# Optimization experiments

Hardware: AMD Instinct MI355X
Metric: run time of the kernel (lower is better)

Reference implementation:

```python
import jax, jax.numpy as jnp
import numpy as np
import math

DN = ('NCHW', 'OIHW', 'NCHW')
TOTAL_STRIDE = 8.0
SCORE_OFFSET = 3.0
SCORE_SIZE = 25
BN_EPS = 1e-5


def conv2d(x, w, b, pad):
    y = jax.lax.conv_general_dilated(x, w, (1, 1), [(pad, pad), (pad, pad)],
                                     dimension_numbers=DN)
    return y + b[None, :, None, None]


def conv_module(x, w1, b1, ws, bs):
    x = conv2d(x, w1, b1, 1)
    for i in range(ws.shape[0]):
        x = conv2d(jax.nn.relu(x), ws[i], bs[i], 1)
    return x


def bn_eval(x, g, b):
    # inference-mode BatchNorm2d: running_mean=0, running_var=1
    s = g / jnp.sqrt(1.0 + BN_EPS)
    return x * s[None, :, None, None] + b[None, :, None, None]


def memory_read(fm, fq):
    B, C, T, H, W = fm.shape
    fm_flat = fm.reshape(B, C, T * H * W)          # (B, C, THW)
    fq_flat = fq.reshape(B, C, H * W)              # (B, C, HW)
    # scores: (B, THW, HW), softmax over the memory axis (THW)
    w = jnp.einsum('bct,bcq->btq', fm_flat, fq_flat) / math.sqrt(512.0)
    w = jax.nn.softmax(w, axis=1)
    mem = jnp.einsum('bct,btq->bcq', fm_flat, w).reshape(B, C, H, W)
    return jnp.concatenate([mem, fq], axis=1)      # (B, 2C, H, W)


def fm_ctr():
    gx = SCORE_OFFSET + TOTAL_STRIDE * jnp.arange(SCORE_SIZE, dtype=jnp.float32)[None, :]
    gy = SCORE_OFFSET + TOTAL_STRIDE * jnp.arange(SCORE_SIZE, dtype=jnp.float32)[:, None]
    return jnp.stack([jnp.broadcast_to(gx, (SCORE_SIZE, SCORE_SIZE)),
                      jnp.broadcast_to(gy, (SCORE_SIZE, SCORE_SIZE))], axis=-1)  # (H,W,2)


def reference(fm, fq, cls1_w, cls1_b, clsk_w, clsk_b, reg1_w, reg1_b, regk_w, regk_b,
              w_cls, b_cls, g_cls, be_cls, w_ctr, b_ctr, g_ctr, be_ctr,
              w_off, b_off, g_off, be_off, si, bi):
    y = memory_read(fm, fq)
    cls_feat = conv_module(y, cls1_w, cls1_b, clsk_w, clsk_b)
    reg_feat = conv_module(y, reg1_w, reg1_b, regk_w, regk_b)
    cls_score = bn_eval(conv2d(cls_feat, w_cls, b_cls, 0), g_cls, be_cls)  # (B,1,H,W)
    ctr_score = bn_eval(conv2d(cls_feat, w_ctr, b_ctr, 0), g_ctr, be_ctr)  # (B,1,H,W)
    offsets = bn_eval(conv2d(reg_feat, w_off, b_off, 0), g_off, be_off)    # (B,4,H,W)

    B = cls_score.shape[0]
    cls_score = cls_score.transpose(0, 2, 3, 1).reshape(B, -1, 1)
    ctr_score = ctr_score.transpose(0, 2, 3, 1).reshape(B, -1, 1)
    offsets = jnp.exp(si * offsets + bi) * TOTAL_STRIDE

    ctr = fm_ctr()                                  # (H,W,2)
    off = offsets.transpose(0, 2, 3, 1)             # (B,H,W,4)
    xy0 = ctr[None] - off[..., :2]
    xy1 = ctr[None] + off[..., 2:]
    bbox = jnp.concatenate([xy0, xy1], axis=-1).reshape(B, -1, 4)
    return cls_score, ctr_score, bbox


def setup_inputs() -> dict:
    key = jax.random.key(0)
    ks = jax.random.split(key, 16)
    B, C, T, H, W = 8, 20, 24, 25, 25
    WSC = 0.02  # small conv-weight scale to keep the 7-conv stack + exp() stable
    inp = {
        'fm': jax.random.normal(ks[0], (B, C, T, H, W), jnp.float32),
        'fq': jax.random.normal(ks[1], (B, C, H, W), jnp.float32),
        'cls1_w': jax.random.normal(ks[2], (256, 40, 3, 3), jnp.float32) * WSC,
        'cls1_b': jnp.zeros((256,), jnp.float32),
        'clsk_w': jax.random.normal(ks[3], (6, 256, 256, 3, 3), jnp.float32) * WSC,
        'clsk_b': jnp.zeros((6, 256), jnp.float32),
        'reg1_w': jax.random.normal(ks[4], (256, 40, 3, 3), jnp.float32) * WSC,
        'reg1_b': jnp.zeros((256,), jnp.float32),
        'regk_w': jax.random.normal(ks[5], (6, 256, 256, 3, 3), jnp.float32) * WSC,
        'regk_b': jnp.zeros((6, 256), jnp.float32),
        'w_cls': jax.random.normal(ks[6], (1, 256, 1, 1), jnp.float32) * WSC,
        'b_cls': jnp.zeros((1,), jnp.float32),
        'g_cls': jnp.ones((1,), jnp.float32),
        'be_cls': jnp.zeros((1,), jnp.float32),
        'w_ctr': jax.random.normal(ks[7], (1, 256, 1, 1), jnp.float32) * WSC,
        'b_ctr': jnp.zeros((1,), jnp.float32),
        'g_ctr': jnp.ones((1,), jnp.float32),
        'be_ctr': jnp.zeros((1,), jnp.float32),
        'w_off': jax.random.normal(ks[8], (4, 256, 1, 1), jnp.float32) * WSC,
        'b_off': jnp.zeros((4,), jnp.float32),
        'g_off': jnp.ones((4,), jnp.float32),
        'be_off': jnp.zeros((4,), jnp.float32),
        'si': jnp.float32(1.0),
        'bi': jnp.float32(0.0),
    }
    return inp
```

## Files before the change

kernel.cpp:

```cpp
#include <hip/hip_runtime.h>
#include <math.h>

#define BATCH 8
#define CCH 20
#define THW 15000
#define HW 625
#define SSIDE 25
#define PHW 729

#define NKEY 15000
#define TPAD 15104
#define NKT 118
#define NKC 20
#define KCHUNK 6

typedef __attribute__((ext_vector_type(8))) short bf16x8;
typedef __attribute__((ext_vector_type(4))) float f32x4;

#define YBF_OFF  0ULL
#define XA_OFF   746496ULL
#define XB_OFF   6718464ULL
#define WT0_OFF  12690432ULL
#define WT_OFF   13280256ULL
#define WTL_ELEMS 1179648ULL
#define FMT_OFF  27436032ULL
#define FM32_OFF 35169280ULL
#define FQB_OFF  42902528ULL
#define PART_OFF 43230208ULL

__device__ __forceinline__ ushort f2bf(float x) {
    unsigned u = __float_as_uint(x);
    u = (u + 0x7FFFu + ((u >> 16) & 1u)) >> 16;
    return (ushort)u;
}
__device__ __forceinline__ float bf2f(ushort v) {
    return __uint_as_float(((unsigned)v) << 16);
}

__device__ __forceinline__ void gload16(const void* g, void* l) {
    __builtin_amdgcn_global_load_lds((const __attribute__((address_space(1))) void*)g,
                                     (__attribute__((address_space(3))) void*)l, 16, 0, 0);
}

__global__ __launch_bounds__(256) void prep_fm(const float* __restrict__ fm,
                                               ushort* __restrict__ fmbT,
                                               ushort* __restrict__ fmb32) {
    __shared__ ushort sT2[256][34];
    const int tid = threadIdx.x;
    const int t0 = blockIdx.x * 256;
    const int b = blockIdx.y;
    const int t = t0 + tid;
    #pragma unroll 4
    for (int c = 0; c < CCH; c++) {
        float v = (t < NKEY) ? fm[((size_t)b * CCH + c) * THW + t] : 0.f;
        ushort h = f2bf(v);
        sT2[tid][c] = h;
        fmb32[((size_t)b * 32 + c) * TPAD + t] = h;
    }
    #pragma unroll
    for (int cz = CCH; cz < 32; cz++)
        fmb32[((size_t)b * 32 + cz) * TPAD + t] = 0;
    __syncthreads();
    const int g = tid >> 4, j = tid & 15;
    uint* dstb = (uint*)fmbT + ((size_t)b * TPAD + t0) * 16 + j;
    #pragma unroll
    for (int i = 0; i < 16; i++) {
        int r = g + 16 * i;
        uint v = 0;
        if (j < 10) v = *(const uint*)&sT2[r][2 * j];
        dstb[(size_t)r * 16] = v;
    }
}

__global__ __launch_bounds__(256) void prep_fq(const float* __restrict__ fq,
                                               ushort* __restrict__ fqb) {
    int idx = blockIdx.x * 256 + threadIdx.x;
    if (idx >= BATCH * 640) return;
    int b = idx / 640, q = idx % 640;
    const float qscale = 1.4426950408889634f * 0.04419417382415922f;
    ushort* dst = fqb + (size_t)idx * 32;
    #pragma unroll 4
    for (int c = 0; c < CCH; c++) {
        float v = (q < HW) ? fq[((size_t)b * CCH + c) * HW + q] * qscale : 0.f;
        dst[c] = f2bf(v);
    }
    #pragma unroll
    for (int c = CCH; c < 32; c++) dst[c] = 0;
}

__global__ __launch_bounds__(512) void attn_flash(const ushort* __restrict__ fmbT,
                                                  const ushort* __restrict__ fmb32,
                                                  const ushort* __restrict__ fqb,
                                                  char* __restrict__ part) {
    __shared__ __align__(16) ushort sK[2][4096];
    __shared__ __align__(16) ushort sV[2][4096];
    __shared__ __align__(16) ushort sP[8][2048];
    const int tid = threadIdx.x;
    const int wave = tid >> 6, lane = tid & 63;
    const int q16 = lane & 15, quad = lane >> 4;
    const int phys = blockIdx.x;
    const int lid = (phys & 7) * 60 + (phys >> 3);
    const int b = lid / 60;
    const int rem = lid - b * 60;
    const int kc = rem / 3;
    const int xq = rem - kc * 3;
    const int qt0 = xq * 2 + (wave >> 2);
    const bool act = (qt0 < 5);
    const int qt = act ? qt0 : 4;
    const int wq = wave & 3;

    bf16x8 Qf[2];
    #pragma unroll
    for (int nf = 0; nf < 2; nf++)
        Qf[nf] = *(const bf16x8*)(fqb + ((size_t)(b * 640 + qt * 128 + wq * 32 + nf * 16 + q16) << 5) + quad * 8);

    f32x4 O[2][2];
    #pragma unroll
    for (int nf = 0; nf < 2; nf++) { O[nf][0] = (f32x4)0.f; O[nf][1] = (f32x4)0.f; }
    float lp0 = 0.f, lp1 = 0.f;
    const f32x4 zz = (f32x4)0.f;

    const int kt0 = kc * KCHUNK;
    const int kt1 = (kt0 + KCHUNK < NKT) ? kt0 + KCHUNK : NKT;

    const int rK = tid >> 2, cK = tid & 3;
    const int rV = tid >> 4, cV = tid & 15;
    const ushort* srcK = fmbT + ((size_t)(b * TPAD + rK) << 5) + ((cK ^ (rK & 3)) << 3);
    const ushort* srcV = fmb32 + (size_t)(b * 32 + rV) * TPAD + ((cV ^ (rV & 7)) << 3);
    auto stage = [&](int kt, int bufi) {
        const int t0s = kt << 7;
        gload16(srcK + ((size_t)t0s << 5), &sK[bufi][wave << 9]);
        gload16(srcV + t0s, &sV[bufi][wave << 9]);
    };

    const int q3 = q16 & 3, q7 = q16 & 7;
    uint* const pBase = (uint*)&sP[wave][q16 << 7];

    int buf = 0;
    stage(kt0, 0);
    for (int kt = kt0; kt < kt1; kt++) {
        if (kt + 1 < kt1) {
            stage(kt + 1, buf ^ 1);
            asm volatile("s_waitcnt vmcnt(2)\n\ts_barrier" ::: "memory");
        } else {
            asm volatile("s_waitcnt vmcnt(0)\n\ts_barrier" ::: "memory");
        }
        const int t0 = kt << 7;
        const bool tail = (t0 + 128 > NKEY);

        bf16x8 Ak[8], Av[8];
        #pragma unroll
        for (int m = 0; m < 8; m++)
            Ak[m] = *(const bf16x8*)&sK[buf][((m * 16 + q16) << 5) + ((quad ^ q3) << 3)];
        #pragma unroll
        for (int mp = 0; mp < 4; mp++)
            #pragma unroll
            for (int cf = 0; cf < 2; cf++)
                Av[mp * 2 + cf] = *(const bf16x8*)&sV[buf][((cf * 16 + q16) << 7) + (((mp * 4 + quad) ^ q7) << 3)];

        f32x4 S[8][2];
        #pragma unroll
        for (int m = 0; m < 8; m++) {
            S[m][0] = __builtin_amdgcn_mfma_f32_16x16x32_bf16(Ak[m], Qf[0], zz, 0, 0, 0);
            S[m][1] = __builtin_amdgcn_mfma_f32_16x16x32_bf16(Ak[m], Qf[1], zz, 0, 0, 0);
        }

        #pragma unroll
        for (int nf = 0; nf < 2; nf++) {
            float lacc = 0.f;
            #pragma unroll
            for (int m = 0; m < 8; m++) {
                float p[4];
                #pragma unroll
                for (int i = 0; i < 4; i++) {
                    float v = __builtin_amdgcn_exp2f(S[m][nf][i]);
                    if (tail && (t0 + m * 16 + quad * 4 + i >= NKEY)) v = 0.f;
                    p[i] = v;
                }
                lacc += (p[0] + p[1]) + (p[2] + p[3]);
                uint pk0 = __builtin_amdgcn_perm(__float_as_uint(p[1]) + 0x8000u,
                                                 __float_as_uint(p[0]) + 0x8000u, 0x07060302u);
                uint pk1 = __builtin_amdgcn_perm(__float_as_uint(p[3]) + 0x8000u,
                                                 __float_as_uint(p[2]) + 0x8000u, 0x07060302u);
                uint* dst = pBase + (((m ^ q7) << 3) + quad * 2);
                dst[0] = pk0;
                dst[1] = pk1;
            }
            if (nf == 0) lp0 += lacc; else lp1 += lacc;
            #pragma unroll
            for (int mp = 0; mp < 4; mp++) {
                bf16x8 Bp = *(const bf16x8*)(pBase + ((mp * 16 + quad * 4) ^ (q7 << 3)));
                O[nf][0] = __builtin_amdgcn_mfma_f32_16x16x32_bf16(Av[mp * 2 + 0], Bp, O[nf][0], 0, 0, 0);
                O[nf][1] = __builtin_amdgcn_mfma_f32_16x16x32_bf16(Av[mp * 2 + 1], Bp, O[nf][1], 0, 0, 0);
            }
        }
        asm volatile("s_waitcnt lgkmcnt(0)\n\ts_barrier" ::: "memory");
        buf ^= 1;
    }

    lp0 += __shfl_xor(lp0, 16); lp0 += __shfl_xor(lp0, 32);
    lp1 += __shfl_xor(lp1, 16); lp1 += __shfl_xor(lp1, 32);

    if (act) {
        #pragma unroll
        for (int nf = 0; nf < 2; nf++) {
            int ql = wq * 32 + nf * 16 + q16;
            size_t rec = ((((size_t)b * 5 + qt) * NKC + kc) * 128 + ql) * 48;
            uint2 pk;
            pk.x = (unsigned)f2bf(O[nf][0][0]) | ((unsigned)f2bf(O[nf][0][1]) << 16);
            pk.y = (unsigned)f2bf(O[nf][0][2]) | ((unsigned)f2bf(O[nf][0][3]) << 16);
            *(uint2*)(part + rec + quad * 8) = pk;
            if (quad == 0) {
                uint2 pk1;
                pk1.x = (unsigned)f2bf(O[nf][1][0]) | ((unsigned)f2bf(O[nf][1][1]) << 16);
                pk1.y = (unsigned)f2bf(O[nf][1][2]) | ((unsigned)f2bf(O[nf][1][3]) << 16);
                *(uint2*)(part + rec + 32) = pk1;
                *(float*)(part + rec + 40) = (nf == 0) ? lp0 : lp1;
            }
        }
    }
}

__device__ __forceinline__ int border_pp(int bi) {
    if (bi < 27) return bi;
    if (bi < 54) return 26 * 27 + (bi - 27);
    if (bi < 79) return (bi - 53) * 27;
    return (bi - 78) * 27 + 26;
}
__global__ __launch_bounds__(256) void attn_merge_zero(const char* __restrict__ part,
                                                       const float* __restrict__ fq,
                                                       ushort* __restrict__ ybf,
                                                       ushort* __restrict__ xa,
                                                       ushort* __restrict__ xb) {
    if (blockIdx.x < 20) {
        int g = blockIdx.x * 256 + threadIdx.x;
        if (g >= BATCH * HW) return;
        int b = g / HW, q = g % HW;
        int qt = q >> 7, ql = q & 127;
        const char* pb = part + ((((size_t)b * 5 + qt) * NKC) * 128 + ql) * 48;
        float L = 0.f;
        float acc[CCH];
        #pragma unroll
        for (int c = 0; c < CCH; c++) acc[c] = 0.f;
        for (int kc = 0; kc < NKC; kc++) {
            const char* rec = pb + (size_t)kc * 128 * 48;
            L += *(const float*)(rec + 40);
            const ushort* av = (const ushort*)rec;
            #pragma unroll
            for (int c = 0; c < CCH; c++) acc[c] += bf2f(av[c]);
        }
        float inv = 1.f / L;
        int pp = (q / 25 + 1) * 27 + (q % 25) + 1;
        ushort* yb = ybf + ((size_t)b * PHW + pp) * 64;
        #pragma unroll
        for (int c = 0; c < CCH; c++) yb[c] = f2bf(acc[c] * inv);
        #pragma unroll
        for (int c = 0; c < CCH; c++) yb[20 + c] = f2bf(fq[((size_t)b * CCH + c) * HW + q]);
        #pragma unroll
        for (int c = 40; c < 64; c++) yb[c] = 0;
    } else {
        int idx = (blockIdx.x - 20) * 256 + threadIdx.x;
        ushort* buf; int cin;
        if (idx < 6656) { buf = ybf; cin = 64; }
        else if (idx < 59904) { idx -= 6656; buf = xa; cin = 256; }
        else if (idx < 113152) { idx -= 59904; buf = xb; cin = 256; }
        else return;
        int nc = cin >> 3;
        int per = 104 * nc;
        int img = idx / per, r = idx - img * per;
        int bi = r / nc, cc = r - bi * nc;
        int pp = border_pp(bi);
        uint4 z = make_uint4(0, 0, 0, 0);
        *(uint4*)&buf[((size_t)img * PHW + pp) * cin + cc * 8] = z;
    }
}

__global__ __launch_bounds__(256) void prep_weights(const float* __restrict__ cw1,
                                                    const float* __restrict__ rw1,
                                                    const float* __restrict__ cwk,
                                                    const float* __restrict__ rwk,
                                                    ushort* __restrict__ wt0,
                                                    ushort* __restrict__ wt) {
    int bid = blockIdx.x;
    if (bid < 1152) {
        int idx = bid * 256 + threadIdx.x;
        if (idx >= 2 * 9 * 256 * 64) return;
        int ic = idx & 63;
        int oc = (idx >> 6) & 255;
        int t = idx >> 14;
        int kyx = t % 9;
        int br = t / 9;
        float v = 0.f;
        if (ic < 40) {
            const float* w = br ? rw1 : cw1;
            v = w[((size_t)oc * 40 + ic) * 9 + kyx];
        }
        wt0[idx] = f2bf(v);
    } else {
        int rb = bid - 1152;
        int s = rb >> 9;
        int idx = (rb & 511) * 256 + threadIdx.x;
        if (idx >= 2 * 256 * 256) return;
        int ic = idx & 255;
        int oc = (idx >> 8) & 255;
        int br = idx >> 16;
        const float* w = br ? rwk : cwk;
        const float* src = w + (((size_t)s * 256 + oc) * 256 + ic) * 9;
        ushort* dst = wt + (size_t)s * WTL_ELEMS;
        float v[9];
        #pragma unroll
        for (int k = 0; k < 9; k++) v[k] = src[k];
        #pragma unroll
        for (int k = 0; k < 9; k++)
            dst[(((size_t)(br * 9 + k)) * 256 + oc) * 256 + ic] = f2bf(v[k]);
    }
}

__global__ __launch_bounds__(256) void conv_gemm(
    const ushort* __restrict__ xin, int cin, int cshift, int in_shared, int relu_out,
    const ushort* __restrict__ wt, const float* __restrict__ bias_c,
    const float* __restrict__ bias_r, ushort* __restrict__ xout) {
    __shared__ __align__(16) ushort sA[3][4096];
    __shared__ __align__(16) ushort sB[3][4096];
    const int tid = threadIdx.x;
    const int lane = tid & 63;
    const int wave = tid >> 6;
    const int n16 = lane & 15, quad = lane >> 4;
    const int wm = wave & 1, wn = wave >> 1;
    const int phys = blockIdx.x;
    const int lid = (phys & 7) * 80 + (phys >> 3);
    const int bb = lid / 40;
    const int rr2 = lid - bb * 40;
    const int ot = rr2 & 3, nt = rr2 >> 2;
    const int oc0 = ot * 64;
    const ushort* wbr = wt + (size_t)(bb < 8 ? 0 : 1) * 9 * 256 * cin;
    const float* bias = (bb < 8) ? bias_c : bias_r;
    const ushort* inb = xin + (size_t)(in_shared ? (bb & 7) : bb) * PHW * cin;

    const int l8 = lane >> 3, j8 = lane & 7;
    const int r0 = wave * 16 + l8;
    const int jj = j8 ^ (l8 & 7);
    const int segA = wave * 1024;

    const ushort* aS0 = wbr + (size_t)(oc0 + r0) * cin + jj * 8;
    const ushort* aS1 = aS0 + (size_t)8 * cin;
    const int p0 = nt * 64 + r0;
    const int p1 = p0 + 8;
    const int pe0 = (p0 < HW) ? p0 : (HW - 1);
    const int pe1 = (p1 < HW) ? p1 : (HW - 1);
    const ushort* bS0 = inb + (size_t)((pe0 / 25) * 27 + (pe0 % 25)) * cin + jj * 8;
    const ushort* bS1 = inb + (size_t)((pe1 / 25) * 27 + (pe1 % 25)) * cin + jj * 8;

    const int NIT = 9 << cshift;
    const int cmask = (1 << cshift) - 1;

    auto issue = [&](int it, int buf) {
        const int kyx = it >> cshift;
        const int ccc = it & cmask;
        const int ky = (kyx >= 6) ? 2 : (kyx >= 3 ? 1 : 0);
        const int kx = kyx - ky * 3;
        const int aoff = kyx * 256 * cin + ccc * 64;
        const int boff = (ky * 27 + kx) * cin + ccc * 64;
        gload16(aS0 + aoff, &sA[buf][segA]);
        gload16(aS1 + aoff, &sA[buf][segA + 512]);
        gload16(bS0 + boff, &sB[buf][segA]);
        gload16(bS1 + boff, &sB[buf][segA + 512]);
    };

    f32x4 acc00 = (f32x4)0.f, acc01 = (f32x4)0.f;
    f32x4 acc10 = (f32x4)0.f, acc11 = (f32x4)0.f;
    const int arow0 = wm * 32 + n16;
    const int brow0 = wn * 32 + n16;
    const int h8 = n16 & 7;

    auto mfma_tile = [&](const ushort* sa, const ushort* sb) {
        #pragma unroll
        for (int ks = 0; ks < 2; ks++) {
            const int swz = ((ks * 4 + quad) ^ h8) * 8;
            bf16x8 a0 = *(const bf16x8*)&sa[arow0 * 64 + swz];
            bf16x8 a1 = *(const bf16x8*)&sa[(arow0 + 16) * 64 + swz];
            bf16x8 b0 = *(const bf16x8*)&sb[brow0 * 64 + swz];
            bf16x8 b1 = *(const bf16x8*)&sb[(brow0 + 16) * 64 + swz];
            acc00 = __builtin_amdgcn_mfma_f32_16x16x32_bf16(a0, b0, acc00, 0, 0, 0);
            acc01 = __builtin_amdgcn_mfma_f32_16x16x32_bf16(a0, b1, acc01, 0, 0, 0);
            acc10 = __builtin_amdgcn_mfma_f32_16x16x32_bf16(a1, b0, acc10, 0, 0, 0);
            acc11 = __builtin_amdgcn_mfma_f32_16x16x32_bf16(a1, b1, acc11, 0, 0, 0);
        }
    };

    issue(0, 0);
    issue(1, 1);
    asm volatile("s_waitcnt vmcnt(4)\n\ts_barrier" ::: "memory");

    for (int it = 0; it < NIT; it += 3) {
        const bool nl = (it + 3 < NIT);
        issue(it + 2, 2);
        mfma_tile(sA[0], sB[0]);
        asm volatile("s_waitcnt vmcnt(4)\n\ts_barrier" ::: "memory");
        if (nl) issue(it + 3, 0);
        mfma_tile(sA[1], sB[1]);
        if (nl) {
            asm volatile("s_waitcnt vmcnt(4)\n\ts_barrier" ::: "memory");
            issue(it + 4, 1);
        } else {
            asm volatile("s_waitcnt vmcnt(0)\n\ts_barrier" ::: "memory");
        }
        mfma_tile(sA[2], sB[2]);
        if (nl) asm volatile("s_waitcnt vmcnt(4)\n\ts_barrier" ::: "memory");
    }

    f32x4 accs[2][2] = {{acc00, acc01}, {acc10, acc11}};
    #pragma unroll
    for (int mf = 0; mf < 2; mf++) {
        int ocb = oc0 + wm * 32 + mf * 16 + quad * 4;
        float4 bv = *(const float4*)(bias + ocb);
        #pragma unroll
        for (int nf = 0; nf < 2; nf++) {
            int pcol = nt * 64 + wn * 32 + nf * 16 + n16;
            if (pcol >= HW) continue;
            int pp = (pcol / 25 + 1) * 27 + (pcol % 25) + 1;
            f32x4 a = accs[mf][nf];
            float v0 = a[0] + bv.x;
            float v1 = a[1] + bv.y;
            float v2 = a[2] + bv.z;
            float v3 = a[3] + bv.w;
            if (relu_out) {
                v0 = fmaxf(v0, 0.f); v1 = fmaxf(v1, 0.f);
                v2 = fmaxf(v2, 0.f); v3 = fmaxf(v3, 0.f);
            }
            uint2 st;
            st.x = (unsigned)f2bf(v0) | ((unsigned)f2bf(v1) << 16);
            st.y = (unsigned)f2bf(v2) | ((unsigned)f2bf(v3) << 16);
            *(uint2*)(&xout[((size_t)bb * PHW + pp) * 256 + ocb]) = st;
        }
    }
}

__global__ __launch_bounds__(256) void heads(const ushort* __restrict__ X,
                                             const float* __restrict__ wcls, const float* __restrict__ bcls,
                                             const float* __restrict__ gcls, const float* __restrict__ becls,
                                             const float* __restrict__ wctr, const float* __restrict__ bctr,
                                             const float* __restrict__ gctr, const float* __restrict__ bectr,
                                             const float* __restrict__ woff, const float* __restrict__ boff,
                                             const float* __restrict__ goff, const float* __restrict__ beoff,
                                             const float* __restrict__ si, const float* __restrict__ bi,
                                             float* __restrict__ out) {
    int g = blockIdx.x * 256 + threadIdx.x;
    if (g >= BATCH * HW) return;
    int b = g / HW, p = g % HW;
    int pp = (p / 25 + 1) * 27 + (p % 25) + 1;
    const ushort* fc = X + ((size_t)b * PHW + pp) * 256;
    const ushort* fr = X + ((size_t)(8 + b) * PHW + pp) * 256;
    float ac = 0.f, at = 0.f, a0 = 0.f, a1 = 0.f, a2 = 0.f, a3 = 0.f;
    for (int c0 = 0; c0 < 256; c0 += 8) {
        uint4 vc = *(const uint4*)(fc + c0);
        uint4 vr = *(const uint4*)(fr + c0);
        unsigned wc_[4] = {vc.x, vc.y, vc.z, vc.w};
        unsigned wr_[4] = {vr.x, vr.y, vr.z, vr.w};
        #pragma unroll
        for (int j = 0; j < 4; j++) {
            float cl = __uint_as_float(wc_[j] << 16);
            float ch = __uint_as_float(wc_[j] & 0xFFFF0000u);
            float rl = __uint_as_float(wr_[j] << 16);
            float rh = __uint_as_float(wr_[j] & 0xFFFF0000u);
            int c = c0 + j * 2;
            ac += wcls[c] * cl + wcls[c + 1] * ch;
            at += wctr[c] * cl + wctr[c + 1] * ch;
            a0 += woff[c] * rl + woff[c + 1] * rh;
            a1 += woff[256 + c] * rl + woff[256 + c + 1] * rh;
            a2 += woff[512 + c] * rl + woff[512 + c + 1] * rh;
            a3 += woff[768 + c] * rl + woff[768 + c + 1] * rh;
        }
    }
    const float bns = 1.f / sqrtf(1.f + 1e-5f);
    float cls = (ac + bcls[0]) * (gcls[0] * bns) + becls[0];
    float ctr = (at + bctr[0]) * (gctr[0] * bns) + bectr[0];
    float sv = si[0], bv = bi[0];
    float o0 = (a0 + boff[0]) * (goff[0] * bns) + beoff[0];
    float o1 = (a1 + boff[1]) * (goff[1] * bns) + beoff[1];
    float o2 = (a2 + boff[2]) * (goff[2] * bns) + beoff[2];
    float o3 = (a3 + boff[3]) * (goff[3] * bns) + beoff[3];
    float e0 = __expf(sv * o0 + bv) * 8.f;
    float e1 = __expf(sv * o1 + bv) * 8.f;
    float e2 = __expf(sv * o2 + bv) * 8.f;
    float e3 = __expf(sv * o3 + bv) * 8.f;
    float gx = 3.f + 8.f * (float)(p % SSIDE);
    float gy = 3.f + 8.f * (float)(p / SSIDE);
    out[g] = cls;
    out[BATCH * HW + g] = ctr;
    float* bbx = out + 2 * BATCH * HW + (size_t)g * 4;
    bbx[0] = gx - e0;
    bbx[1] = gy - e1;
    bbx[2] = gx + e2;
    bbx[3] = gy + e3;
}

extern "C" void kernel_launch(void* const* d_in, const int* in_sizes, int n_in,
                              void* d_out, int out_size, void* d_ws, size_t ws_size,
                              hipStream_t stream) {
    const float* fm     = (const float*)d_in[0];
    const float* fq     = (const float*)d_in[1];
    const float* cls1_w = (const float*)d_in[2];
    const float* cls1_b = (const float*)d_in[3];
    const float* clsk_w = (const float*)d_in[4];
    const float* clsk_b = (const float*)d_in[5];
    const float* reg1_w = (const float*)d_in[6];
    const float* reg1_b = (const float*)d_in[7];
    const float* regk_w = (const float*)d_in[8];
    const float* regk_b = (const float*)d_in[9];
    const float* w_cls  = (const float*)d_in[10];
    const float* b_cls  = (const float*)d_in[11];
    const float* g_cls  = (const float*)d_in[12];
    const float* be_cls = (const float*)d_in[13];
    const float* w_ctr  = (const float*)d_in[14];
    const float* b_ctr  = (const float*)d_in[15];
    const float* g_ctr  = (const float*)d_in[16];
    const float* be_ctr = (const float*)d_in[17];
    const float* w_off  = (const float*)d_in[18];
    const float* b_off  = (const float*)d_in[19];
    const float* g_off  = (const float*)d_in[20];
    const float* be_off = (const float*)d_in[21];
    const float* si     = (const float*)d_in[22];
    const float* bi     = (const float*)d_in[23];

    char* ws = (char*)d_ws;
    ushort* YBF  = (ushort*)(ws + YBF_OFF);
    ushort* XA   = (ushort*)(ws + XA_OFF);
    ushort* XB   = (ushort*)(ws + XB_OFF);
    ushort* WT0  = (ushort*)(ws + WT0_OFF);
    ushort* WT   = (ushort*)(ws + WT_OFF);
    ushort* FMT  = (ushort*)(ws + FMT_OFF);
    ushort* FM32 = (ushort*)(ws + FM32_OFF);
    ushort* FQB  = (ushort*)(ws + FQB_OFF);
    char*   PART = ws + PART_OFF;

    prep_fm<<<dim3(59, 8), 256, 0, stream>>>(fm, FMT, FM32);
    prep_fq<<<dim3(20), 256, 0, stream>>>(fq, FQB);
    attn_flash<<<dim3(480), 512, 0, stream>>>(FMT, FM32, FQB, PART);
    attn_merge_zero<<<dim3(462), 256, 0, stream>>>(PART, fq, YBF, XA, XB);

    prep_weights<<<dim3(1152 + 512 * 6), 256, 0, stream>>>(cls1_w, reg1_w, clsk_w, regk_w, WT0, WT);

    conv_gemm<<<dim3(640), 256, 0, stream>>>(YBF, 64, 0, 1, 1, WT0, cls1_b, reg1_b, XA);

    ushort* cur = XA;
    ushort* nxt = XB;
    for (int s = 0; s < 6; s++) {
        int relu_out = (s < 5) ? 1 : 0;
        conv_gemm<<<dim3(640), 256, 0, stream>>>(cur, 256, 2, 0, relu_out,
            WT + (size_t)s * WTL_ELEMS,
            clsk_b + (size_t)s * 256, regk_b + (size_t)s * 256, nxt);
        ushort* tmp = cur; cur = nxt; nxt = tmp;
    }

    heads<<<dim3(20), 256, 0, stream>>>(cur, w_cls, b_cls, g_cls, be_cls,
                                        w_ctr, b_ctr, g_ctr, be_ctr,
                                        w_off, b_off, g_off, be_off, si, bi,
                                        (float*)d_out);
}
```

Before: 360.8 us.

## Split-K the 3x3 conv GEMMs into two halves with a separate combine kernel

Replaces each of the six 256->256 conv layers with a split-K GEMM that partitions the 36 K-iterations (9 taps x 4 channel chunks) into two halves, launching 1280 blocks instead of 640, each writing fp32 partials. A new combine kernel sums the two partials, adds bias, applies ReLU and writes padded bf16 output. The goal is to fill more CUs and shorten the per-block K loop on a small-M/N problem. In exchange it adds extra fp32 partial traffic (about 10MB per layer) and one more kernel launch per layer.

```diff
diff --git a/kernel.cpp b/kernel.cpp
--- a/kernel.cpp
+++ b/kernel.cpp
@@ -27,6 +27,7 @@
 #define FM32_OFF 35169280ULL
 #define FQB_OFF  42902528ULL
 #define PART_OFF 43230208ULL
+#define PC_OFF   48145408ULL
 
 __device__ __forceinline__ ushort f2bf(float x) {
     unsigned u = __float_as_uint(x);
@@ -436,6 +437,154 @@
     }
 }
 
+__global__ __launch_bounds__(256) void conv_gemm_sk(
+    const ushort* __restrict__ xin, const ushort* __restrict__ wt,
+    float* __restrict__ pout) {
+    __shared__ __align__(16) ushort sA[3][4096];
+    __shared__ __align__(16) ushort sB[3][4096];
+    const int cin = 256;
+    const int tid = threadIdx.x;
+    const int lane = tid & 63;
+    const int wave = tid >> 6;
+    const int n16 = lane & 15, quad = lane >> 4;
+    const int wm = wave & 1, wn = wave >> 1;
+    const int phys = blockIdx.x;
+    const int lid = (phys & 7) * 160 + (phys >> 3);
+    const int kh = lid / 640;
+    const int l2 = lid - kh * 640;
+    const int bb = l2 / 40;
+    const int rr2 = l2 - bb * 40;
+    const int ot = rr2 & 3, nt = rr2 >> 2;
+    const int oc0 = ot * 64;
+    const ushort* wbr = wt + (size_t)(bb < 8 ? 0 : 1) * 9 * 256 * cin;
+    const ushort* inb = xin + (size_t)bb * PHW * cin;
+
+    const int l8 = lane >> 3, j8 = lane & 7;
+    const int r0 = wave * 16 + l8;
+    const int jj = j8 ^ (l8 & 7);
+    const int segA = wave * 1024;
+
+    const ushort* aS0 = wbr + (size_t)(oc0 + r0) * cin + jj * 8;
+    const ushort* aS1 = aS0 + (size_t)8 * cin;
+    const int p0 = nt * 64 + r0;
+    const int p1 = p0 + 8;
+    const int pe0 = (p0 < HW) ? p0 : (HW - 1);
+    const int pe1 = (p1 < HW) ? p1 : (HW - 1);
+    const ushort* bS0 = inb + (size_t)((pe0 / 25) * 27 + (pe0 % 25)) * cin + jj * 8;
+    const ushort* bS1 = inb + (size_t)((pe1 / 25) * 27 + (pe1 % 25)) * cin + jj * 8;
+
+    const int it0 = kh * 18;
+
+    auto issue = [&](int it, int buf) {
+        const int kyx = it >> 2;
+        const int ccc = it & 3;
+        const int ky = (kyx >= 6) ? 2 : (kyx >= 3 ? 1 : 0);
+        const int kx = kyx - ky * 3;
+        const int aoff = kyx * 256 * cin + ccc * 64;
+        const int boff = (ky * 27 + kx) * cin + ccc * 64;
+        gload16(aS0 + aoff, &sA[buf][segA]);
+        gload16(aS1 + aoff, &sA[buf][segA + 512]);
+        gload16(bS0 + boff, &sB[buf][segA]);
+        gload16(bS1 + boff, &sB[buf][segA + 512]);
+    };
+
+    f32x4 acc00 = (f32x4)0.f, acc01 = (f32x4)0.f;
+    f32x4 acc10 = (f32x4)0.f, acc11 = (f32x4)0.f;
+    const int arow0 = wm * 32 + n16;
+    const int brow0 = wn * 32 + n16;
+    const int h8 = n16 & 7;
+
+    auto mfma_tile = [&](const ushort* sa, const ushort* sb) {
+        #pragma unroll
+        for (int ks = 0; ks < 2; ks++) {
+            const int swz = ((ks * 4 + quad) ^ h8) * 8;
+            bf16x8 a0 = *(const bf16x8*)&sa[arow0 * 64 + swz];
+            bf16x8 a1 = *(const bf16x8*)&sa[(arow0 + 16) * 64 + swz];
+            bf16x8 b0 = *(const bf16x8*)&sb[brow0 * 64 + swz];
+            bf16x8 b1 = *(const bf16x8*)&sb[(brow0 + 16) * 64 + swz];
+            acc00 = __builtin_amdgcn_mfma_f32_16x16x32_bf16(a0, b0, acc00, 0, 0, 0);
+            acc01 = __builtin_amdgcn_mfma_f32_16x16x32_bf16(a0, b1, acc01, 0, 0, 0);
+            acc10 = __builtin_amdgcn_mfma_f32_16x16x32_bf16(a1, b0, acc10, 0, 0, 0);
+            acc11 = __builtin_amdgcn_mfma_f32_16x16x32_bf16(a1, b1, acc11, 0, 0, 0);
+        }
+    };
+
+    issue(it0 + 0, 0);
+    issue(it0 + 1, 1);
+    asm volatile("s_waitcnt vmcnt(4)\n\ts_barrier" ::: "memory");
+
+    for (int k = 0; k < 18; k += 3) {
+        const bool nl = (k + 3 < 18);
+        issue(it0 + k + 2, 2);
+        mfma_tile(sA[0], sB[0]);
+        asm volatile("s_waitcnt vmcnt(4)\n\ts_barrier" ::: "memory");
+        if (nl) issue(it0 + k + 3, 0);
+        mfma_tile(sA[1], sB[1]);
+        if (nl) {
+            asm volatile("s_waitcnt vmcnt(4)\n\ts_barrier" ::: "memory");
+            issue(it0 + k + 4, 1);
+        } else {
+            asm volatile("s_waitcnt vmcnt(0)\n\ts_barrier" ::: "memory");
+        }
+        mfma_tile(sA[2], sB[2]);
+        if (nl) asm volatile("s_waitcnt vmcnt(4)\n\ts_barrier" ::: "memory");
+    }
+
+    float* pbase = pout + (size_t)kh * 16 * HW * 256;
+    f32x4 accs[2][2] = {{acc00, acc01}, {acc10, acc11}};
+    #pragma unroll
+    for (int mf = 0; mf < 2; mf++) {
+        int ocb = oc0 + wm * 32 + mf * 16 + quad * 4;
+        #pragma unroll
+        for (int nf = 0; nf < 2; nf++) {
+            int pcol = nt * 64 + wn * 32 + nf * 16 + n16;
+            if (pcol >= HW) continue;
+            f32x4 a = accs[mf][nf];
+            *(float4*)(pbase + ((size_t)bb * HW + pcol) * 256 + ocb) =
+                make_float4(a[0], a[1], a[2], a[3]);
+        }
+    }
+}
+
+__global__ __launch_bounds__(256) void conv_combine(const float* __restrict__ pc,
+                                                    const float* __restrict__ bias_c,
+                                                    const float* __restrict__ bias_r,
+                                                    int relu_out,
+                                                    ushort* __restrict__ xout) {
+    int g = blockIdx.x * 256 + threadIdx.x;
+    if (g >= 16 * HW * 32) return;
+    int oc8 = (g & 31) * 8;
+    int rest = g >> 5;
+    int p = rest % HW;
+    int b = rest / HW;
+    size_t i0 = ((size_t)b * HW + p) * 256 + oc8;
+    const float* p0 = pc + i0;
+    const float* p1 = pc + (size_t)16 * HW * 256 + i0;
+    const float* bias = ((b < 8) ? bias_c : bias_r) + oc8;
+    float4 x0 = *(const float4*)p0;
+    float4 x1 = *(const float4*)(p0 + 4);
+    float4 y0 = *(const float4*)p1;
+    float4 y1 = *(const float4*)(p1 + 4);
+    float4 b0 = *(const float4*)bias;
+    float4 b1 = *(const float4*)(bias + 4);
+    float v[8];
+    v[0] = x0.x + y0.x + b0.x; v[1] = x0.y + y0.y + b0.y;
+    v[2] = x0.z + y0.z + b0.z; v[3] = x0.w + y0.w + b0.w;
+    v[4] = x1.x + y1.x + b1.x; v[5] = x1.y + y1.y + b1.y;
+    v[6] = x1.z + y1.z + b1.z; v[7] = x1.w + y1.w + b1.w;
+    if (relu_out) {
+        #pragma unroll
+        for (int j = 0; j < 8; j++) v[j] = fmaxf(v[j], 0.f);
+    }
+    uint4 st;
+    st.x = (unsigned)f2bf(v[0]) | ((unsigned)f2bf(v[1]) << 16);
+    st.y = (unsigned)f2bf(v[2]) | ((unsigned)f2bf(v[3]) << 16);
+    st.z = (unsigned)f2bf(v[4]) | ((unsigned)f2bf(v[5]) << 16);
+    st.w = (unsigned)f2bf(v[6]) | ((unsigned)f2bf(v[7]) << 16);
+    int pp = (p / 25 + 1) * 27 + (p % 25) + 1;
+    *(uint4*)&xout[((size_t)b * PHW + pp) * 256 + oc8] = st;
+}
+
 __global__ __launch_bounds__(256) void heads(const ushort* __restrict__ X,
                                              const float* __restrict__ wcls, const float* __restrict__ bcls,
                                              const float* __restrict__ gcls, const float* __restrict__ becls,
@@ -533,6 +682,7 @@
     ushort* FM32 = (ushort*)(ws + FM32_OFF);
     ushort* FQB  = (ushort*)(ws + FQB_OFF);
     char*   PART = ws + PART_OFF;
+    float*  PC   = (float*)(ws + PC_OFF);
 
     prep_fm<<<dim3(59, 8), 256, 0, stream>>>(fm, FMT, FM32);
     prep_fq<<<dim3(20), 256, 0, stream>>>(fq, FQB);
@@ -547,9 +697,9 @@
     ushort* nxt = XB;
     for (int s = 0; s < 6; s++) {
         int relu_out = (s < 5) ? 1 : 0;
-        conv_gemm<<<dim3(640), 256, 0, stream>>>(cur, 256, 2, 0, relu_out,
-            WT + (size_t)s * WTL_ELEMS,
-            clsk_b + (size_t)s * 256, regk_b + (size_t)s * 256, nxt);
+        conv_gemm_sk<<<dim3(1280), 256, 0, stream>>>(cur, WT + (size_t)s * WTL_ELEMS, PC);
+        conv_combine<<<dim3(1250), 256, 0, stream>>>(PC, clsk_b + (size_t)s * 256,
+                                                     regk_b + (size_t)s * 256, relu_out, nxt);
         ushort* tmp = cur; cur = nxt; nxt = tmp;
     }
 
```

New measurement: 414.7 us. 15.0% more time.
